# Performance work log

Measured on AMD Instinct MI355X. Metric: run time of the kernel, lower is better.

The kernel has to match this reference:

```python
import jax, jax.numpy as jnp
import numpy as np
from jax import lax

B, T, H, IN = 1024, 100, 512, 4  # batch, seq len (fixed 100 in source), hidden, nucleotide dim


def _lstm_cell(x, h, c, Wih, Whh, b):
    # PyTorch gate order: i, f, g, o ; b = b_ih + b_hh
    gates = x @ Wih.T + h @ Whh.T + b
    i, f, g, o = jnp.split(gates, 4, axis=-1)
    c = jax.nn.sigmoid(f) * c + jax.nn.sigmoid(i) * jnp.tanh(g)
    h = jax.nn.sigmoid(o) * jnp.tanh(c)
    return h, c


def _run_layer(xs, Wih, Whh, b):
    # xs: [T, B, in] -> ys: [T, B, H], final (h, c)
    Bn = xs.shape[1]
    h0 = jnp.zeros((Bn, H), xs.dtype)
    c0 = jnp.zeros((Bn, H), xs.dtype)

    def step(carry, x):
        h, c = carry
        h, c = _lstm_cell(x, h, c, Wih, Whh, b)
        return (h, c), h

    (h, c), ys = lax.scan(step, (h0, c0), xs)
    return ys, h, c


def setup_inputs() -> dict:
    key = jax.random.key(0)
    ks = jax.random.split(key, 16)
    s = lambda fan: 1.0 / np.sqrt(fan)

    def W(k, shape, fan):
        return jax.random.uniform(k, shape, jnp.float32, -s(fan), s(fan))

    inp = {
        "X": jax.random.normal(ks[0], (B, T, IN), jnp.float32),
        "epoch": 10,
        # encoder LSTM (2 layers)
        "enc_Wih0": W(ks[1], (4 * H, IN), H),
        "enc_Whh0": W(ks[2], (4 * H, H), H),
        "enc_b0": jnp.zeros((4 * H,), jnp.float32),
        "enc_Wih1": W(ks[3], (4 * H, H), H),
        "enc_Whh1": W(ks[4], (4 * H, H), H),
        "enc_b1": jnp.zeros((4 * H,), jnp.float32),
        # decoder LSTM (2 layers, input dim = seq_in_dim = 4)
        "dec_Wih0": W(ks[5], (4 * H, IN), H),
        "dec_Whh0": W(ks[6], (4 * H, H), H),
        "dec_b0": jnp.zeros((4 * H,), jnp.float32),
        "dec_Wih1": W(ks[7], (4 * H, H), H),
        "dec_Whh1": W(ks[8], (4 * H, H), H),
        "dec_b1": jnp.zeros((4 * H,), jnp.float32),
        # predict_MLP = Linear(H, 4)
        "Wp": W(ks[9], (IN, H), H),
        "bp": jnp.zeros((IN,), jnp.float32),
    }
    return inp


def reference(X, epoch, enc_Wih0, enc_Whh0, enc_b0, enc_Wih1, enc_Whh1, enc_b1,
              dec_Wih0, dec_Whh0, dec_b0, dec_Wih1, dec_Whh1, dec_b1, Wp, bp):
    # ---- Encoder: 2-layer LSTM over X (batch_first -> scan over time) ----
    xs = jnp.swapaxes(X, 0, 1)  # [T, B, 4]
    ys0, h0e, c0e = _run_layer(xs, enc_Wih0, enc_Whh0, enc_b0)
    _, h1e, c1e = _run_layer(ys0, enc_Wih1, enc_Whh1, enc_b1)

    #      discretize_input=False) ----
    Bn = X.shape[0]
    x_init = jnp.zeros((Bn, IN), X.dtype)

    def dec_step(carry, _):
        x, h0, c0, h1, c1 = carry
        h0, c0 = _lstm_cell(x, h0, c0, dec_Wih0, dec_Whh0, dec_b0)
        h1, c1 = _lstm_cell(h0, h1, c1, dec_Wih1, dec_Whh1, dec_b1)
        pred = h1 @ Wp.T + bp                 # [B, 4] logits
        x_next = jax.nn.softmax(pred, axis=-1)
        return (x_next, h0, c0, h1, c1), pred

    _, preds = lax.scan(dec_step, (x_init, h0e, c0e, h1e, c1e), None, length=T)
    # out_seq list of [B,1,4] in torch -> stacked [B, 100, 4]
    return jnp.swapaxes(preds, 0, 1)
```

## Files before the change

kernel.cpp:

```cpp
#include <hip/hip_runtime.h>
#include <math.h>
#include <stdint.h>

typedef _Float16 f16;
typedef _Float16 f16x8 __attribute__((ext_vector_type(8)));
typedef float f32x4 __attribute__((ext_vector_type(4)));

#define BATCH 1024
#define HD    512
#define TST   100
#define BUFSZ 49152

__device__ __forceinline__ float4 coh_ld_x4(const void* p) {
    float4 v;
    asm volatile("global_load_dwordx4 %0, %1, off sc0 sc1" : "=v"(v) : "v"(p) : "memory");
    return v;
}
__device__ __forceinline__ float4 ld_x4(const void* p) {
    float4 v;
    asm volatile("global_load_dwordx4 %0, %1, off" : "=v"(v) : "v"(p) : "memory");
    return v;
}
__device__ __forceinline__ void coh_store_u32(uint32_t* p, uint32_t v) {
    asm volatile("global_store_dword %0, %1, off sc0 sc1" :: "v"(p), "v"(v) : "memory");
}
__device__ __forceinline__ void coh_store_i32(int* p, int v) {
    asm volatile("global_store_dword %0, %1, off sc0 sc1" :: "v"(p), "v"(v) : "memory");
}
__device__ __forceinline__ int coh_load_i32(const int* p) {
    int v;
    asm volatile("global_load_dword %0, %1, off sc0 sc1\n\ts_waitcnt vmcnt(0)"
                 : "=v"(v) : "v"(p) : "memory");
    return v;
}
__device__ __forceinline__ void drain_vm() {
    asm volatile("s_waitcnt vmcnt(0)" ::: "memory");
    __builtin_amdgcn_sched_barrier(0);
}
__device__ __forceinline__ void wait_vm(int n) {
    switch (n) {
    case 0:  asm volatile("s_waitcnt vmcnt(0)"  ::: "memory"); break;
    case 8:  asm volatile("s_waitcnt vmcnt(8)"  ::: "memory"); break;
    case 12: asm volatile("s_waitcnt vmcnt(12)" ::: "memory"); break;
    case 16: asm volatile("s_waitcnt vmcnt(16)" ::: "memory"); break;
    default: asm volatile("s_waitcnt vmcnt(20)" ::: "memory"); break;
    }
    __builtin_amdgcn_sched_barrier(0);
}

__device__ __forceinline__ float fast_sig(float x) {
    return 1.0f / (1.0f + __expf(-x));
}
__device__ __forceinline__ float fast_tanh(float x) {
    float xc = fminf(fmaxf(x, -15.0f), 15.0f);
    float e = __expf(2.0f * xc);
    return 1.0f - 2.0f / (e + 1.0f);
}

__global__ void split_w(const float* __restrict__ src0, int ksplit,
                        const float* __restrict__ src1, int NKT, f16* __restrict__ out)
{
    int c = blockIdx.x * 256 + threadIdx.x;
    int total = 16 * NKT * 2048;
    if (c >= total) return;
    int u = c & 2047;
    int t2 = c >> 11;
    int kt = t2 % NKT;
    int mt = t2 / NKT;
    int line = u >> 4;
    int s = (u & 15) ^ (line & 15);
    int plane = s >> 3, o = s & 7;
    int m = mt * 128 + line;
    int row = (m & 3) * HD + (m >> 2);
    int kb = kt * 64 + o * 8;
    f16 v[8];
    #pragma unroll
    for (int e = 0; e < 8; ++e) {
        int k = kb + e;
        float w = (k < ksplit) ? src0[(size_t)row * ksplit + k]
                               : src1[(size_t)row * HD + (k - ksplit)];
        float w32 = w * 32.0f;
        f16 hi = (f16)w32;
        v[e] = plane ? (f16)((w32 - (float)hi) * 2048.0f) : hi;
    }
    *(f16x8*)(out + (size_t)c * 8) = *(f16x8*)v;
}

__global__ void prep_b4(const float* __restrict__ b, float* __restrict__ bt) {
    int c = blockIdx.x * 256 + threadIdx.x;
    if (c < 2048) bt[c] = b[(c & 3) * HD + (c >> 2)];
}

__global__ void prep_wih4(const float* __restrict__ W, float* __restrict__ o) {
    int c = blockIdx.x * 256 + threadIdx.x;
    if (c < 8192) {
        int j = c & 3, g = (c >> 2) & 3, hl = c >> 4;
        o[c] = W[(size_t)(g * HD + hl) * 4 + j];
    }
}

__device__ __forceinline__ void publish(int* cell, int epoch) {
    drain_vm();
    __syncthreads();
    if (threadIdx.x == 0)
        coh_store_i32(cell, epoch);
}

__device__ __forceinline__ void wait2(const int* a, int ta, const int* b, int tb) {
    if (threadIdx.x < 64) {
        const int l = threadIdx.x & 15;
        const bool useB = (threadIdx.x & 16) != 0;
        const int* p = (useB ? b : a) + l * 16;
        const int tgt = useB ? tb : ta;
        for (;;) {
            int v = coh_load_i32(p);
            if (__all(v >= tgt)) break;
            __builtin_amdgcn_s_sleep(2);
        }
    }
    __syncthreads();
}

template<int NKT, bool RANK4>
__device__ __forceinline__ void layer_step(
    const f16* __restrict__ Wst, const f16* __restrict__ src1, const f16* __restrict__ src2,
    const float* __restrict__ wih4, const float* __restrict__ xin, int xstride,
    const float* __restrict__ bt4, float* __restrict__ cT, f16* __restrict__ hout,
    char* smem, int mt, int nt)
{
    const int tid = threadIdx.x;
    const int lane = tid & 63;
    const int wv = tid >> 6;
    const int wm = wv & 1, wn = wv >> 1;
    const int l15 = lane & 15, j = lane >> 4;
    const int n0 = nt * 64;

    const int q = (j ^ l15) << 4;
    int ALr[4], BLb[2];
    #pragma unroll
    for (int f = 0; f < 4; ++f) ALr[f] = (wm * 64 + f * 16 + l15) * 256;
    #pragma unroll
    for (int fn = 0; fn < 2; ++fn) BLb[fn] = 32768 + (wn * 32 + fn * 16 + l15) * 256;

    float4 rak[2][8];
    float4 rbk[4][4];
    float4 xv[2];

    auto issueA = [&](int kt, int bank) {
        const f16* ga = Wst + ((size_t)mt * NKT + kt) * 2048 * 8;
        #pragma unroll
        for (int i = 0; i < 8; ++i)
            rak[bank][i] = ld_x4(ga + (size_t)(i * 256 + tid) * 8);
    };
    auto issueB = [&](int kt, int bank) {
        #pragma unroll
        for (int i = 0; i < 4; ++i) {
            int v = i * 256 + tid;
            int line = v >> 4;
            int s = (v & 15) ^ (line & 15);
            int ks = kt * 64 + (s & 7) * 8;
            const f16* sp = src1; int kl = ks;
            if (NKT == 16 && ks >= 512) { sp = src2; kl = ks - 512; }
            rbk[bank][i] = coh_ld_x4(sp + (size_t)(n0 + line) * 1024 + (s >> 3) * 512 + kl);
        }
    };

    f32x4 accA[4][2] = {};
    f32x4 accB[4][2] = {};

    if (RANK4) {
        #pragma unroll
        for (int fn = 0; fn < 2; ++fn) {
            const int n = n0 + wn * 32 + fn * 16 + l15;
            xv[fn] = coh_ld_x4(xin + (size_t)n * xstride);
        }
    }
    issueB(0, 0); issueA(0, 0); issueB(1, 1); issueA(1, 1); issueB(2, 2); issueB(3, 3);

    #pragma unroll
    for (int kt = 0; kt < NKT; ++kt) {
        char* buf = smem + (kt & 1) * BUFSZ;
        const int wcnt = (kt == NKT - 1) ? 0 : (kt == NKT - 2) ? 8 :
                         (kt == NKT - 3) ? 12 : (kt <= 1) ? 20 : 16;
        wait_vm(wcnt);
        #pragma unroll
        for (int i = 0; i < 8; ++i) *(float4*)(buf + (i * 256 + tid) * 16) = rak[kt & 1][i];
        #pragma unroll
        for (int i = 0; i < 4; ++i) *(float4*)(buf + 32768 + (i * 256 + tid) * 16) = rbk[kt & 3][i];
        if (kt + 2 < NKT) issueA(kt + 2, kt & 1);
        if (kt + 4 < NKT) issueB(kt + 4, kt & 3);
        __syncthreads();
        #pragma unroll
        for (int i = 0; i < 2; ++i) {
            const int off = (i << 6) ^ q;
            f16x8 ah[4], al[4], bh[2], bl[2];
            #pragma unroll
            for (int f = 0; f < 4; ++f) {
                ah[f] = *(const f16x8*)(buf + ALr[f] + off);
                al[f] = *(const f16x8*)(buf + ALr[f] + (off ^ 0x80));
            }
            #pragma unroll
            for (int fn = 0; fn < 2; ++fn) {
                bh[fn] = *(const f16x8*)(buf + BLb[fn] + off);
                bl[fn] = *(const f16x8*)(buf + BLb[fn] + (off ^ 0x80));
            }
            #pragma unroll
            for (int f = 0; f < 4; ++f)
                #pragma unroll
                for (int fn = 0; fn < 2; ++fn) {
                    accA[f][fn] = __builtin_amdgcn_mfma_f32_16x16x32_f16(ah[f], bh[fn], accA[f][fn], 0, 0, 0);
                    accB[f][fn] = __builtin_amdgcn_mfma_f32_16x16x32_f16(al[f], bh[fn], accB[f][fn], 0, 0, 0);
                    accB[f][fn] = __builtin_amdgcn_mfma_f32_16x16x32_f16(ah[f], bl[fn], accB[f][fn], 0, 0, 0);
                }
        }
    }

    const float sA = 1.0f / 1024.0f;
    const float sB = 1.0f / (1024.0f * 2048.0f);

    uint32_t* htile = (uint32_t*)smem;
    #pragma unroll
    for (int f = 0; f < 4; ++f) {
        const int hl_loc = wm * 16 + f * 4 + j;
        const int hl = mt * 32 + hl_loc;
        const float4 bv = *(const float4*)(bt4 + hl * 4);
        #pragma unroll
        for (int fn = 0; fn < 2; ++fn) {
            const int n_loc = wn * 32 + fn * 16 + l15;
            const int n = n0 + n_loc;
            float g0 = accA[f][fn][0] * sA + accB[f][fn][0] * sB + bv.x;
            float g1 = accA[f][fn][1] * sA + accB[f][fn][1] * sB + bv.y;
            float g2 = accA[f][fn][2] * sA + accB[f][fn][2] * sB + bv.z;
            float g3 = accA[f][fn][3] * sA + accB[f][fn][3] * sB + bv.w;
            if (RANK4) {
                const float4* wr = (const float4*)(wih4 + hl * 16);
                const float4 x4 = xv[fn];
                g0 += wr[0].x * x4.x + wr[0].y * x4.y + wr[0].z * x4.z + wr[0].w * x4.w;
                g1 += wr[1].x * x4.x + wr[1].y * x4.y + wr[1].z * x4.z + wr[1].w * x4.w;
                g2 += wr[2].x * x4.x + wr[2].y * x4.y + wr[2].z * x4.z + wr[2].w * x4.w;
                g3 += wr[3].x * x4.x + wr[3].y * x4.y + wr[3].z * x4.z + wr[3].w * x4.w;
            }
            const size_t co = (size_t)hl * 1024 + n;
            const float cold = cT[co];
            const float si = fast_sig(g0);
            const float sf = fast_sig(g1);
            const float so = fast_sig(g3);
            const float cn = sf * cold + si * fast_tanh(g2);
            const float hn = so * fast_tanh(cn);
            cT[co] = cn;
            const float h32 = hn * 32.0f;
            const f16 hi = (f16)h32;
            const f16 lo = (f16)((h32 - (float)hi) * 2048.0f);
            uint32_t pk = ((uint32_t)__builtin_bit_cast(uint16_t, lo) << 16)
                        | (uint32_t)__builtin_bit_cast(uint16_t, hi);
            htile[n_loc * 33 + hl_loc] = pk;
        }
    }
    __syncthreads();
    uint32_t* h32out = (uint32_t*)hout;
    #pragma unroll
    for (int i = 0; i < 8; ++i) {
        int u = i * 256 + tid;
        int n_loc = u >> 5;
        int r = u & 31;
        int plane = r >> 4;
        int p = r & 15;
        uint32_t t0 = htile[n_loc * 33 + 2 * p];
        uint32_t t1 = htile[n_loc * 33 + 2 * p + 1];
        uint32_t w = plane ? ((t1 & 0xffff0000u) | (t0 >> 16))
                           : ((t1 << 16) | (t0 & 0xffffu));
        coh_store_u32(h32out + (size_t)(n0 + n_loc) * 512 + plane * 256 + mt * 16 + p, w);
    }
}

__device__ __forceinline__ void pred_step(
    const f16* __restrict__ h1, const float* __restrict__ Wp, const float* __restrict__ bp,
    float* __restrict__ outp, float* __restrict__ xfb, int t, int mt, int nt)
{
    const int lane = threadIdx.x & 63;
    const int wv = threadIdx.x >> 6;
    const int n = nt * 64 + mt * 4 + wv;
    const f16* hr = h1 + (size_t)n * 1024;
    const int k0 = lane * 8;
    float4 hv4 = coh_ld_x4(hr + k0);
    float4 lv4 = coh_ld_x4(hr + 512 + k0);
    drain_vm();
    f16x8 hv = __builtin_bit_cast(f16x8, hv4);
    f16x8 lv = __builtin_bit_cast(f16x8, lv4);
    float h[8];
    #pragma unroll
    for (int e = 0; e < 8; ++e)
        h[e] = (float)hv[e] * 0.03125f + (float)lv[e] * (1.0f / 65536.0f);
    float a[4] = {};
    #pragma unroll
    for (int g = 0; g < 4; ++g) {
        const float4 wa = *(const float4*)(Wp + g * HD + k0);
        const float4 wb = *(const float4*)(Wp + g * HD + k0 + 4);
        a[g] = h[0]*wa.x + h[1]*wa.y + h[2]*wa.z + h[3]*wa.w
             + h[4]*wb.x + h[5]*wb.y + h[6]*wb.z + h[7]*wb.w;
    }
    #pragma unroll
    for (int off = 32; off > 0; off >>= 1) {
        a[0] += __shfl_xor(a[0], off);
        a[1] += __shfl_xor(a[1], off);
        a[2] += __shfl_xor(a[2], off);
        a[3] += __shfl_xor(a[3], off);
    }
    if (lane == 0) {
        const float4 bv = *(const float4*)bp;
        float v0 = a[0] + bv.x, v1 = a[1] + bv.y, v2 = a[2] + bv.z, v3 = a[3] + bv.w;
        float* op = outp + (size_t)n * (TST * 4) + t * 4;
        op[0] = v0; op[1] = v1; op[2] = v2; op[3] = v3;
        float m = fmaxf(fmaxf(v0, v1), fmaxf(v2, v3));
        float e0 = expf(v0 - m), e1 = expf(v1 - m), e2 = expf(v2 - m), e3 = expf(v3 - m);
        float inv = 1.0f / (e0 + e1 + e2 + e3);
        uint32_t* xp = (uint32_t*)(xfb + n * 4);
        float s0 = e0 * inv, s1 = e1 * inv, s2 = e2 * inv, s3 = e3 * inv;
        coh_store_u32(xp + 0, __builtin_bit_cast(uint32_t, s0));
        coh_store_u32(xp + 1, __builtin_bit_cast(uint32_t, s1));
        coh_store_u32(xp + 2, __builtin_bit_cast(uint32_t, s2));
        coh_store_u32(xp + 3, __builtin_bit_cast(uint32_t, s3));
    }
}

struct Params {
    const f16 *WE0, *WE1, *WD0, *WD1;
    const float *wih4E, *wih4D, *btE0, *btE1, *btD0, *btD1;
    const float *X, *Wp, *bp;
    f16 *h0a, *h0b, *h1a, *h1b;
    float *c0, *c1;
    float *xfb0, *xfb1;
    float *out;
    int *f0, *f1, *fp;
};

__launch_bounds__(256, 1) __global__ void lstm_persistent(Params P)
{
    __shared__ __align__(16) char smem[2 * BUFSZ];
    const int bx = blockIdx.x;
    const int mt = ((bx & 7) << 1) | ((bx >> 3) & 1);
    const int nt = bx >> 4;
    int* f0g = P.f0 + nt * 256;
    int* f1g = P.f1 + nt * 256;
    int* fpg = P.fp + nt * 256;
    int* my0 = f0g + mt * 16;
    int* my1 = f1g + mt * 16;
    int* myp = fpg + mt * 16;
    f16* h0b_[2] = { P.h0a, P.h0b };
    f16* h1b_[2] = { P.h1a, P.h1b };
    float* xfb_[2] = { P.xfb0, P.xfb1 };

    for (int u = 0; u < 2 * TST; ++u) {
        const bool enc = (u < TST);
        const int t = enc ? u : u - TST;

        if (enc) wait2(f0g, u, f0g, u);
        else     wait2(f0g, u, fpg, t);
        layer_step<8, true>(enc ? P.WE0 : P.WD0,
                            h0b_[(u + 1) & 1], nullptr,
                            enc ? P.wih4E : P.wih4D,
                            enc ? (P.X + t * 4) : xfb_[(t + 1) & 1],
                            enc ? (TST * 4) : 4,
                            enc ? P.btE0 : P.btD0,
                            P.c0, h0b_[u & 1], smem, mt, nt);
        publish(my0, u + 1);

        wait2(f0g, u + 1, f1g, u);
        layer_step<16, false>(enc ? P.WE1 : P.WD1,
                              h0b_[u & 1], h1b_[(u + 1) & 1],
                              nullptr, nullptr, 0,
                              enc ? P.btE1 : P.btD1,
                              P.c1, h1b_[u & 1], smem, mt, nt);
        publish(my1, u + 1);

        if (!enc) {
            wait2(f1g, u + 1, f1g, u + 1);
            pred_step(h1b_[u & 1], P.Wp, P.bp, P.out, xfb_[t & 1], t, mt, nt);
            publish(myp, t + 1);
        }
    }
}

extern "C" void kernel_launch(void* const* d_in, const int* in_sizes, int n_in,
                              void* d_out, int out_size, void* d_ws, size_t ws_size,
                              hipStream_t stream)
{
    const float* X     = (const float*)d_in[0];
    const float* eWih0 = (const float*)d_in[2];
    const float* eWhh0 = (const float*)d_in[3];
    const float* eb0   = (const float*)d_in[4];
    const float* eWih1 = (const float*)d_in[5];
    const float* eWhh1 = (const float*)d_in[6];
    const float* eb1   = (const float*)d_in[7];
    const float* dWih0 = (const float*)d_in[8];
    const float* dWhh0 = (const float*)d_in[9];
    const float* db0   = (const float*)d_in[10];
    const float* dWih1 = (const float*)d_in[11];
    const float* dWhh1 = (const float*)d_in[12];
    const float* db1   = (const float*)d_in[13];
    const float* Wp    = (const float*)d_in[14];
    const float* bp    = (const float*)d_in[15];

    char* ws = (char*)d_ws;
    size_t off = 0;
    auto alloc = [&](size_t bytes) { char* p = ws + off; off += (bytes + 255) & ~(size_t)255; return p; };
    f16* WE0 = (f16*)alloc((size_t)16 * 8  * 2048 * 16);
    f16* WE1 = (f16*)alloc((size_t)16 * 16 * 2048 * 16);
    f16* WD0 = (f16*)alloc((size_t)16 * 8  * 2048 * 16);
    f16* WD1 = (f16*)alloc((size_t)16 * 16 * 2048 * 16);
    float* wih4E = (float*)alloc(8192 * 4);
    float* wih4D = (float*)alloc(8192 * 4);
    float* btE0 = (float*)alloc(2048 * 4);
    float* btE1 = (float*)alloc(2048 * 4);
    float* btD0 = (float*)alloc(2048 * 4);
    float* btD1 = (float*)alloc(2048 * 4);
    f16* h0a = (f16*)alloc((size_t)BATCH * 1024 * 2);
    f16* h0b = (f16*)alloc((size_t)BATCH * 1024 * 2);
    f16* h1a = (f16*)alloc((size_t)BATCH * 1024 * 2);
    f16* h1b = (f16*)alloc((size_t)BATCH * 1024 * 2);
    float* c0  = (float*)alloc((size_t)HD * BATCH * 4);
    float* c1  = (float*)alloc((size_t)HD * BATCH * 4);
    float* xfb0 = (float*)alloc((size_t)BATCH * 4 * 4);
    float* xfb1 = (float*)alloc((size_t)BATCH * 4 * 4);
    int* f0 = (int*)alloc(16 * 256 * 4);
    int* f1 = (int*)alloc(16 * 256 * 4);
    int* fp = (int*)alloc(16 * 256 * 4);
    if (off > ws_size) return;

    split_w<<<(16 * 8  * 2048) / 256, 256, 0, stream>>>(nullptr, 0,   eWhh0, 8,  WE0);
    split_w<<<(16 * 16 * 2048) / 256, 256, 0, stream>>>(eWih1, 512, eWhh1, 16, WE1);
    split_w<<<(16 * 8  * 2048) / 256, 256, 0, stream>>>(nullptr, 0,   dWhh0, 8,  WD0);
    split_w<<<(16 * 16 * 2048) / 256, 256, 0, stream>>>(dWih1, 512, dWhh1, 16, WD1);
    prep_wih4<<<32, 256, 0, stream>>>(eWih0, wih4E);
    prep_wih4<<<32, 256, 0, stream>>>(dWih0, wih4D);
    prep_b4<<<8, 256, 0, stream>>>(eb0, btE0);
    prep_b4<<<8, 256, 0, stream>>>(eb1, btE1);
    prep_b4<<<8, 256, 0, stream>>>(db0, btD0);
    prep_b4<<<8, 256, 0, stream>>>(db1, btD1);

    hipMemsetAsync(h0b, 0, (size_t)BATCH * 1024 * 2, stream);
    hipMemsetAsync(h1b, 0, (size_t)BATCH * 1024 * 2, stream);
    hipMemsetAsync(c0, 0, (size_t)HD * BATCH * 4, stream);
    hipMemsetAsync(c1, 0, (size_t)HD * BATCH * 4, stream);
    hipMemsetAsync(xfb1, 0, (size_t)BATCH * 4 * 4, stream);
    hipMemsetAsync(f0, 0, 16 * 256 * 4, stream);
    hipMemsetAsync(f1, 0, 16 * 256 * 4, stream);
    hipMemsetAsync(fp, 0, 16 * 256 * 4, stream);

    Params P;
    P.WE0 = WE0; P.WE1 = WE1; P.WD0 = WD0; P.WD1 = WD1;
    P.wih4E = wih4E; P.wih4D = wih4D;
    P.btE0 = btE0; P.btE1 = btE1; P.btD0 = btD0; P.btD1 = btD1;
    P.X = X; P.Wp = Wp; P.bp = bp;
    P.h0a = h0a; P.h0b = h0b; P.h1a = h1a; P.h1b = h1b;
    P.c0 = c0; P.c1 = c1;
    P.xfb0 = xfb0; P.xfb1 = xfb1;
    P.out = (float*)d_out;
    P.f0 = f0; P.f1 = f1; P.fp = fp;

    lstm_persistent<<<256, 256, 0, stream>>>(P);

    (void)in_sizes; (void)n_in; (void)out_size;
}
```

Before: 7.382 ms.

## Retile persistent LSTM to 256x32 tiles with 32x32 MFMA and direct-register weights

Changes the per-block tile from 128 gate rows x 64 batch columns to 256 gate rows x 32 batch columns, using 32x32x16 MFMA instructions. Weight fragments are now loaded from global memory straight into registers in MFMA-ready order, so they no longer pass through shared memory. Only the h operand is staged in a small double-buffered LDS region. Weight pre-layout, flag indexing, the grid mapping and the projection indexing are all rewritten to match. This cuts LDS traffic and LDS footprint per step, but every block now streams twice as many weight rows through registers, and the hand-tuned vmcnt waits must stay exactly right.

```diff
diff --git a/kernel.cpp b/kernel.cpp
--- a/kernel.cpp
+++ b/kernel.cpp
@@ -4,12 +4,11 @@
 
 typedef _Float16 f16;
 typedef _Float16 f16x8 __attribute__((ext_vector_type(8)));
-typedef float f32x4 __attribute__((ext_vector_type(4)));
+typedef float f32x16 __attribute__((ext_vector_type(16)));
 
 #define BATCH 1024
 #define HD    512
 #define TST   100
-#define BUFSZ 49152
 
 __device__ __forceinline__ float4 coh_ld_x4(const void* p) {
     float4 v;
@@ -40,10 +39,12 @@
 __device__ __forceinline__ void wait_vm(int n) {
     switch (n) {
     case 0:  asm volatile("s_waitcnt vmcnt(0)"  ::: "memory"); break;
-    case 8:  asm volatile("s_waitcnt vmcnt(8)"  ::: "memory"); break;
-    case 12: asm volatile("s_waitcnt vmcnt(12)" ::: "memory"); break;
-    case 16: asm volatile("s_waitcnt vmcnt(16)" ::: "memory"); break;
-    default: asm volatile("s_waitcnt vmcnt(20)" ::: "memory"); break;
+    case 4:  asm volatile("s_waitcnt vmcnt(4)"  ::: "memory"); break;
+    case 6:  asm volatile("s_waitcnt vmcnt(6)"  ::: "memory"); break;
+    case 10: asm volatile("s_waitcnt vmcnt(10)" ::: "memory"); break;
+    case 26: asm volatile("s_waitcnt vmcnt(26)" ::: "memory"); break;
+    case 32: asm volatile("s_waitcnt vmcnt(32)" ::: "memory"); break;
+    default: asm volatile("s_waitcnt vmcnt(34)" ::: "memory"); break;
     }
     __builtin_amdgcn_sched_barrier(0);
 }
@@ -61,27 +62,27 @@
                         const float* __restrict__ src1, int NKT, f16* __restrict__ out)
 {
     int c = blockIdx.x * 256 + threadIdx.x;
-    int total = 16 * NKT * 2048;
+    int total = 8 * NKT * 4096;
     if (c >= total) return;
-    int u = c & 2047;
-    int t2 = c >> 11;
+    int q = c & 4095;
+    int t2 = c >> 12;
     int kt = t2 % NKT;
     int mt = t2 / NKT;
-    int line = u >> 4;
-    int s = (u & 15) ^ (line & 15);
-    int plane = s >> 3, o = s & 7;
-    int m = mt * 128 + line;
-    int row = (m & 3) * HD + (m >> 2);
-    int kb = kt * 64 + o * 8;
+    int inner = q >> 8;
+    int row = q & 255;
+    int s = inner >> 2, p = (inner >> 1) & 1, half = inner & 1;
+    int m = mt * 256 + row;
+    int orow = (m & 3) * HD + (m >> 2);
+    int kb = kt * 64 + s * 16 + half * 8;
     f16 v[8];
     #pragma unroll
     for (int e = 0; e < 8; ++e) {
         int k = kb + e;
-        float w = (k < ksplit) ? src0[(size_t)row * ksplit + k]
-                               : src1[(size_t)row * HD + (k - ksplit)];
+        float w = (k < ksplit) ? src0[(size_t)orow * ksplit + k]
+                               : src1[(size_t)orow * HD + (k - ksplit)];
         float w32 = w * 32.0f;
         f16 hi = (f16)w32;
-        v[e] = plane ? (f16)((w32 - (float)hi) * 2048.0f) : hi;
+        v[e] = p ? (f16)((w32 - (float)hi) * 2048.0f) : hi;
     }
     *(f16x8*)(out + (size_t)c * 8) = *(f16x8*)v;
 }
@@ -108,8 +109,8 @@
 
 __device__ __forceinline__ void wait2(const int* a, int ta, const int* b, int tb) {
     if (threadIdx.x < 64) {
-        const int l = threadIdx.x & 15;
-        const bool useB = (threadIdx.x & 16) != 0;
+        const int l = threadIdx.x & 7;
+        const bool useB = (threadIdx.x & 8) != 0;
         const int* p = (useB ? b : a) + l * 16;
         const int tgt = useB ? tb : ta;
         for (;;) {
@@ -128,118 +129,122 @@
     const float* __restrict__ bt4, float* __restrict__ cT, f16* __restrict__ hout,
     char* smem, int mt, int nt)
 {
-    const int tid = threadIdx.x;
+    const int tid  = threadIdx.x;
     const int lane = tid & 63;
-    const int wv = tid >> 6;
-    const int wm = wv & 1, wn = wv >> 1;
-    const int l15 = lane & 15, j = lane >> 4;
-    const int n0 = nt * 64;
-
-    const int q = (j ^ l15) << 4;
-    int ALr[4], BLb[2];
-    #pragma unroll
-    for (int f = 0; f < 4; ++f) ALr[f] = (wm * 64 + f * 16 + l15) * 256;
-    #pragma unroll
-    for (int fn = 0; fn < 2; ++fn) BLb[fn] = 32768 + (wn * 32 + fn * 16 + l15) * 256;
-
-    float4 rak[2][8];
-    float4 rbk[4][4];
-    float4 xv[2];
-
-    auto issueA = [&](int kt, int bank) {
-        const f16* ga = Wst + ((size_t)mt * NKT + kt) * 2048 * 8;
-        #pragma unroll
-        for (int i = 0; i < 8; ++i)
-            rak[bank][i] = ld_x4(ga + (size_t)(i * 256 + tid) * 8);
+    const int wv   = tid >> 6;
+    const int col  = lane & 31;
+    const int half = lane >> 5;
+    const int xk   = lane & 15;
+    const int n0   = nt * 32;
+
+    const size_t tbaseA = (size_t)half * 4096 + (size_t)(wv * 64 + col) * 16;
+    const int colb = col * 256;
+
+    float4 ab0[4], ab1[4], ab2[4], ab3[4];
+    float4 rb0[2], rb1[2];
+    float4 xv = make_float4(0.f, 0.f, 0.f, 0.f);
+
+    auto issueA = [&](int kt, int s, float4 (&bank)[4]) {
+        const char* ga = (const char*)Wst + ((size_t)(mt * NKT + kt) << 16)
+                       + ((size_t)s << 14) + tbaseA;
+        bank[0] = ld_x4(ga);
+        bank[1] = ld_x4(ga + 8192);
+        bank[2] = ld_x4(ga + 512);
+        bank[3] = ld_x4(ga + 8704);
     };
-    auto issueB = [&](int kt, int bank) {
-        #pragma unroll
-        for (int i = 0; i < 4; ++i) {
-            int v = i * 256 + tid;
-            int line = v >> 4;
-            int s = (v & 15) ^ (line & 15);
-            int ks = kt * 64 + (s & 7) * 8;
-            const f16* sp = src1; int kl = ks;
-            if (NKT == 16 && ks >= 512) { sp = src2; kl = ks - 512; }
-            rbk[bank][i] = coh_ld_x4(sp + (size_t)(n0 + line) * 1024 + (s >> 3) * 512 + kl);
-        }
-    };
-
-    f32x4 accA[4][2] = {};
-    f32x4 accB[4][2] = {};
-
-    if (RANK4) {
-        #pragma unroll
-        for (int fn = 0; fn < 2; ++fn) {
-            const int n = n0 + wn * 32 + fn * 16 + l15;
-            xv[fn] = coh_ld_x4(xin + (size_t)n * xstride);
-        }
-    }
-    issueB(0, 0); issueA(0, 0); issueB(1, 1); issueA(1, 1); issueB(2, 2); issueB(3, 3);
-
-    #pragma unroll
-    for (int kt = 0; kt < NKT; ++kt) {
-        char* buf = smem + (kt & 1) * BUFSZ;
-        const int wcnt = (kt == NKT - 1) ? 0 : (kt == NKT - 2) ? 8 :
-                         (kt == NKT - 3) ? 12 : (kt <= 1) ? 20 : 16;
-        wait_vm(wcnt);
-        #pragma unroll
-        for (int i = 0; i < 8; ++i) *(float4*)(buf + (i * 256 + tid) * 16) = rak[kt & 1][i];
-        #pragma unroll
-        for (int i = 0; i < 4; ++i) *(float4*)(buf + 32768 + (i * 256 + tid) * 16) = rbk[kt & 3][i];
-        if (kt + 2 < NKT) issueA(kt + 2, kt & 1);
-        if (kt + 4 < NKT) issueB(kt + 4, kt & 3);
-        __syncthreads();
+    auto issueB = [&](int kt, float4 (&rb)[2]) {
         #pragma unroll
         for (int i = 0; i < 2; ++i) {
-            const int off = (i << 6) ^ q;
-            f16x8 ah[4], al[4], bh[2], bl[2];
-            #pragma unroll
-            for (int f = 0; f < 4; ++f) {
-                ah[f] = *(const f16x8*)(buf + ALr[f] + off);
-                al[f] = *(const f16x8*)(buf + ALr[f] + (off ^ 0x80));
-            }
-            #pragma unroll
-            for (int fn = 0; fn < 2; ++fn) {
-                bh[fn] = *(const f16x8*)(buf + BLb[fn] + off);
-                bl[fn] = *(const f16x8*)(buf + BLb[fn] + (off ^ 0x80));
-            }
-            #pragma unroll
-            for (int f = 0; f < 4; ++f)
-                #pragma unroll
-                for (int fn = 0; fn < 2; ++fn) {
-                    accA[f][fn] = __builtin_amdgcn_mfma_f32_16x16x32_f16(ah[f], bh[fn], accA[f][fn], 0, 0, 0);
-                    accB[f][fn] = __builtin_amdgcn_mfma_f32_16x16x32_f16(al[f], bh[fn], accB[f][fn], 0, 0, 0);
-                    accB[f][fn] = __builtin_amdgcn_mfma_f32_16x16x32_f16(ah[f], bl[fn], accB[f][fn], 0, 0, 0);
-                }
-        }
+            int u = i * 256 + tid;
+            int bc = u >> 4, w16 = u & 15;
+            int si = w16 ^ (bc & 15);
+            int p = si >> 3;
+            int kh = kt * 64 + ((si >> 1) & 3) * 16 + (si & 1) * 8;
+            const f16* sp = src1; int kl = kh;
+            if (NKT == 16 && kh >= 512) { sp = src2; kl = kh - 512; }
+            rb[i] = coh_ld_x4(sp + (size_t)(n0 + bc) * 1024 + p * 512 + kl);
+        }
+    };
+
+    f32x16 accA0 = {}, accA1 = {}, accB0 = {}, accB1 = {};
+
+    if (RANK4) xv = coh_ld_x4(xin + (size_t)(n0 + col) * xstride);
+    issueB(0, rb0);
+    issueB(1, rb1);
+    issueA(0, 0, ab0);
+    issueA(0, 1, ab1);
+
+    #pragma unroll
+    for (int kt = 0; kt < NKT; ++kt) {
+        char* buf = smem + (kt & 1) * 8192;
+        wait_vm(kt == 0 ? 10 : kt == 1 ? 26 : kt == NKT - 1 ? 32 : 34);
+        if ((kt & 1) == 0) {
+            *(float4*)(buf + tid * 16)        = rb0[0];
+            *(float4*)(buf + 4096 + tid * 16) = rb0[1];
+            if (kt + 2 < NKT) issueB(kt + 2, rb0);
+        } else {
+            *(float4*)(buf + tid * 16)        = rb1[0];
+            *(float4*)(buf + 4096 + tid * 16) = rb1[1];
+            if (kt + 2 < NKT) issueB(kt + 2, rb1);
+        }
+        __syncthreads();
+
+        #define KSTEP(S, BK)                                                              \
+        {                                                                                 \
+            f16x8 bh = *(const f16x8*)(buf + colb + ((((S) * 2 + half) ^ xk) << 4));       \
+            f16x8 bl = *(const f16x8*)(buf + colb + (((8 + (S) * 2 + half) ^ xk) << 4));   \
+            f16x8 ah0 = __builtin_bit_cast(f16x8, BK[0]);                                 \
+            f16x8 al0 = __builtin_bit_cast(f16x8, BK[1]);                                 \
+            f16x8 ah1 = __builtin_bit_cast(f16x8, BK[2]);                                 \
+            f16x8 al1 = __builtin_bit_cast(f16x8, BK[3]);                                 \
+            accA0 = __builtin_amdgcn_mfma_f32_32x32x16_f16(ah0, bh, accA0, 0, 0, 0);      \
+            accB0 = __builtin_amdgcn_mfma_f32_32x32x16_f16(al0, bh, accB0, 0, 0, 0);      \
+            accB0 = __builtin_amdgcn_mfma_f32_32x32x16_f16(ah0, bl, accB0, 0, 0, 0);      \
+            accA1 = __builtin_amdgcn_mfma_f32_32x32x16_f16(ah1, bh, accA1, 0, 0, 0);      \
+            accB1 = __builtin_amdgcn_mfma_f32_32x32x16_f16(al1, bh, accB1, 0, 0, 0);      \
+            accB1 = __builtin_amdgcn_mfma_f32_32x32x16_f16(ah1, bl, accB1, 0, 0, 0);      \
+        }
+
+        wait_vm(kt >= NKT - 2 ? 4 : 6);
+        KSTEP(0, ab0)
+        issueA(kt, 2, ab2);
+        wait_vm(kt >= NKT - 2 ? 4 : 6);
+        KSTEP(1, ab1)
+        issueA(kt, 3, ab3);
+        wait_vm(4);
+        KSTEP(2, ab2)
+        if (kt + 1 < NKT) issueA(kt + 1, 0, ab0);
+        wait_vm(kt == NKT - 1 ? 0 : 4);
+        KSTEP(3, ab3)
+        if (kt + 1 < NKT) issueA(kt + 1, 1, ab1);
+        #undef KSTEP
     }
 
     const float sA = 1.0f / 1024.0f;
     const float sB = 1.0f / (1024.0f * 2048.0f);
-
-    uint32_t* htile = (uint32_t*)smem;
-    #pragma unroll
-    for (int f = 0; f < 4; ++f) {
-        const int hl_loc = wm * 16 + f * 4 + j;
-        const int hl = mt * 32 + hl_loc;
-        const float4 bv = *(const float4*)(bt4 + hl * 4);
+    uint32_t* htile = (uint32_t*)(smem + 16384);
+
+    #pragma unroll
+    for (int f = 0; f < 2; ++f) {
+        const f32x16 aA = f ? accA1 : accA0;
+        const f32x16 aB = f ? accB1 : accB0;
         #pragma unroll
-        for (int fn = 0; fn < 2; ++fn) {
-            const int n_loc = wn * 32 + fn * 16 + l15;
-            const int n = n0 + n_loc;
-            float g0 = accA[f][fn][0] * sA + accB[f][fn][0] * sB + bv.x;
-            float g1 = accA[f][fn][1] * sA + accB[f][fn][1] * sB + bv.y;
-            float g2 = accA[f][fn][2] * sA + accB[f][fn][2] * sB + bv.z;
-            float g3 = accA[f][fn][3] * sA + accB[f][fn][3] * sB + bv.w;
+        for (int qq = 0; qq < 4; ++qq) {
+            const int hl_loc = wv * 16 + f * 8 + 2 * qq + half;
+            const int hl = mt * 64 + hl_loc;
+            const float4 bv = *(const float4*)(bt4 + hl * 4);
+            float g0 = aA[4 * qq + 0] * sA + aB[4 * qq + 0] * sB + bv.x;
+            float g1 = aA[4 * qq + 1] * sA + aB[4 * qq + 1] * sB + bv.y;
+            float g2 = aA[4 * qq + 2] * sA + aB[4 * qq + 2] * sB + bv.z;
+            float g3 = aA[4 * qq + 3] * sA + aB[4 * qq + 3] * sB + bv.w;
             if (RANK4) {
                 const float4* wr = (const float4*)(wih4 + hl * 16);
-                const float4 x4 = xv[fn];
-                g0 += wr[0].x * x4.x + wr[0].y * x4.y + wr[0].z * x4.z + wr[0].w * x4.w;
-                g1 += wr[1].x * x4.x + wr[1].y * x4.y + wr[1].z * x4.z + wr[1].w * x4.w;
-                g2 += wr[2].x * x4.x + wr[2].y * x4.y + wr[2].z * x4.z + wr[2].w * x4.w;
-                g3 += wr[3].x * x4.x + wr[3].y * x4.y + wr[3].z * x4.z + wr[3].w * x4.w;
+                g0 += wr[0].x * xv.x + wr[0].y * xv.y + wr[0].z * xv.z + wr[0].w * xv.w;
+                g1 += wr[1].x * xv.x + wr[1].y * xv.y + wr[1].z * xv.z + wr[1].w * xv.w;
+                g2 += wr[2].x * xv.x + wr[2].y * xv.y + wr[2].z * xv.z + wr[2].w * xv.w;
+                g3 += wr[3].x * xv.x + wr[3].y * xv.y + wr[3].z * xv.z + wr[3].w * xv.w;
             }
+            const int n = n0 + col;
             const size_t co = (size_t)hl * 1024 + n;
             const float cold = cT[co];
             const float si = fast_sig(g0);
@@ -248,28 +253,28 @@
             const float cn = sf * cold + si * fast_tanh(g2);
             const float hn = so * fast_tanh(cn);
             cT[co] = cn;
-            const float h32 = hn * 32.0f;
-            const f16 hi = (f16)h32;
-            const f16 lo = (f16)((h32 - (float)hi) * 2048.0f);
+            const float h32v = hn * 32.0f;
+            const f16 hi = (f16)h32v;
+            const f16 lo = (f16)((h32v - (float)hi) * 2048.0f);
             uint32_t pk = ((uint32_t)__builtin_bit_cast(uint16_t, lo) << 16)
                         | (uint32_t)__builtin_bit_cast(uint16_t, hi);
-            htile[n_loc * 33 + hl_loc] = pk;
+            htile[col * 65 + hl_loc] = pk;
         }
     }
     __syncthreads();
     uint32_t* h32out = (uint32_t*)hout;
     #pragma unroll
-    for (int i = 0; i < 8; ++i) {
-        int u = i * 256 + tid;
-        int n_loc = u >> 5;
-        int r = u & 31;
-        int plane = r >> 4;
-        int p = r & 15;
-        uint32_t t0 = htile[n_loc * 33 + 2 * p];
-        uint32_t t1 = htile[n_loc * 33 + 2 * p + 1];
-        uint32_t w = plane ? ((t1 & 0xffff0000u) | (t0 >> 16))
+    for (int e = 0; e < 8; ++e) {
+        int u = e * 256 + tid;
+        int cc = u >> 6;
+        int rem = u & 63;
+        int pl = rem >> 5;
+        int w = rem & 31;
+        uint32_t t0 = htile[cc * 65 + 2 * w];
+        uint32_t t1 = htile[cc * 65 + 2 * w + 1];
+        uint32_t word = pl ? ((t1 & 0xffff0000u) | (t0 >> 16))
                            : ((t1 << 16) | (t0 & 0xffffu));
-        coh_store_u32(h32out + (size_t)(n0 + n_loc) * 512 + plane * 256 + mt * 16 + p, w);
+        coh_store_u32(h32out + (size_t)(n0 + cc) * 512 + pl * 256 + mt * 32 + w, word);
     }
 }
 
@@ -279,7 +284,7 @@
 {
     const int lane = threadIdx.x & 63;
     const int wv = threadIdx.x >> 6;
-    const int n = nt * 64 + mt * 4 + wv;
+    const int n = nt * 32 + mt * 4 + wv;
     const f16* hr = h1 + (size_t)n * 1024;
     const int k0 = lane * 8;
     float4 hv4 = coh_ld_x4(hr + k0);
@@ -336,13 +341,13 @@
 
 __launch_bounds__(256, 1) __global__ void lstm_persistent(Params P)
 {
-    __shared__ __align__(16) char smem[2 * BUFSZ];
+    __shared__ __align__(16) char smem[16384 + 8448];
     const int bx = blockIdx.x;
-    const int mt = ((bx & 7) << 1) | ((bx >> 3) & 1);
-    const int nt = bx >> 4;
-    int* f0g = P.f0 + nt * 256;
-    int* f1g = P.f1 + nt * 256;
-    int* fpg = P.fp + nt * 256;
+    const int mt = bx & 7;
+    const int nt = bx >> 3;
+    int* f0g = P.f0 + nt * 128;
+    int* f1g = P.f1 + nt * 128;
+    int* fpg = P.fp + nt * 128;
     int* my0 = f0g + mt * 16;
     int* my1 = f1g + mt * 16;
     int* myp = fpg + mt * 16;
@@ -404,10 +409,10 @@
     char* ws = (char*)d_ws;
     size_t off = 0;
     auto alloc = [&](size_t bytes) { char* p = ws + off; off += (bytes + 255) & ~(size_t)255; return p; };
-    f16* WE0 = (f16*)alloc((size_t)16 * 8  * 2048 * 16);
-    f16* WE1 = (f16*)alloc((size_t)16 * 16 * 2048 * 16);
-    f16* WD0 = (f16*)alloc((size_t)16 * 8  * 2048 * 16);
-    f16* WD1 = (f16*)alloc((size_t)16 * 16 * 2048 * 16);
+    f16* WE0 = (f16*)alloc((size_t)8 * 8  * 65536);
+    f16* WE1 = (f16*)alloc((size_t)8 * 16 * 65536);
+    f16* WD0 = (f16*)alloc((size_t)8 * 8  * 65536);
+    f16* WD1 = (f16*)alloc((size_t)8 * 16 * 65536);
     float* wih4E = (float*)alloc(8192 * 4);
     float* wih4D = (float*)alloc(8192 * 4);
     float* btE0 = (float*)alloc(2048 * 4);
@@ -422,15 +427,15 @@
     float* c1  = (float*)alloc((size_t)HD * BATCH * 4);
     float* xfb0 = (float*)alloc((size_t)BATCH * 4 * 4);
     float* xfb1 = (float*)alloc((size_t)BATCH * 4 * 4);
-    int* f0 = (int*)alloc(16 * 256 * 4);
-    int* f1 = (int*)alloc(16 * 256 * 4);
-    int* fp = (int*)alloc(16 * 256 * 4);
+    int* f0 = (int*)alloc(32 * 128 * 4);
+    int* f1 = (int*)alloc(32 * 128 * 4);
+    int* fp = (int*)alloc(32 * 128 * 4);
     if (off > ws_size) return;
 
-    split_w<<<(16 * 8  * 2048) / 256, 256, 0, stream>>>(nullptr, 0,   eWhh0, 8,  WE0);
-    split_w<<<(16 * 16 * 2048) / 256, 256, 0, stream>>>(eWih1, 512, eWhh1, 16, WE1);
-    split_w<<<(16 * 8  * 2048) / 256, 256, 0, stream>>>(nullptr, 0,   dWhh0, 8,  WD0);
-    split_w<<<(16 * 16 * 2048) / 256, 256, 0, stream>>>(dWih1, 512, dWhh1, 16, WD1);
+    split_w<<<(8 * 8  * 4096) / 256, 256, 0, stream>>>(nullptr, 0,   eWhh0, 8,  WE0);
+    split_w<<<(8 * 16 * 4096) / 256, 256, 0, stream>>>(eWih1, 512, eWhh1, 16, WE1);
+    split_w<<<(8 * 8  * 4096) / 256, 256, 0, stream>>>(nullptr, 0,   dWhh0, 8,  WD0);
+    split_w<<<(8 * 16 * 4096) / 256, 256, 0, stream>>>(dWih1, 512, dWhh1, 16, WD1);
     prep_wih4<<<32, 256, 0, stream>>>(eWih0, wih4E);
     prep_wih4<<<32, 256, 0, stream>>>(dWih0, wih4D);
     prep_b4<<<8, 256, 0, stream>>>(eb0, btE0);
@@ -443,9 +448,9 @@
     hipMemsetAsync(c0, 0, (size_t)HD * BATCH * 4, stream);
     hipMemsetAsync(c1, 0, (size_t)HD * BATCH * 4, stream);
     hipMemsetAsync(xfb1, 0, (size_t)BATCH * 4 * 4, stream);
-    hipMemsetAsync(f0, 0, 16 * 256 * 4, stream);
-    hipMemsetAsync(f1, 0, 16 * 256 * 4, stream);
-    hipMemsetAsync(fp, 0, 16 * 256 * 4, stream);
+    hipMemsetAsync(f0, 0, 32 * 128 * 4, stream);
+    hipMemsetAsync(f1, 0, 32 * 128 * 4, stream);
+    hipMemsetAsync(fp, 0, 32 * 128 * 4, stream);
 
     Params P;
     P.WE0 = WE0; P.WE1 = WE1; P.WD0 = WD0; P.WD1 = WD1;
```

Measured after the change: 7.458 ms. No clear change (+1.0%).

## Halve batch tile and K-chunk to run 512 persistent blocks at two per CU

Applied to the files above, without the earlier changes.

Each persistent block now covers 32 batch columns instead of 64 and walks K in 32-wide chunks instead of 64. The weight staging layout, shared buffers and prefetch depth shrink to match, and the grid doubles to 512 blocks with two resident per CU. The goal is more parallelism and latency hiding across CUs for the serial recurrent steps. In exchange each weight tile is streamed twice as often, the flag arrays grow, and more blocks take part in every grid-wide synchronisation.

```diff
diff --git a/kernel.cpp b/kernel.cpp
--- a/kernel.cpp
+++ b/kernel.cpp
@@ -9,7 +9,7 @@
 #define BATCH 1024
 #define HD    512
 #define TST   100
-#define BUFSZ 49152
+#define BUFSZ 20480
 
 __device__ __forceinline__ float4 coh_ld_x4(const void* p) {
     float4 v;
@@ -38,13 +38,8 @@
     __builtin_amdgcn_sched_barrier(0);
 }
 __device__ __forceinline__ void wait_vm(int n) {
-    switch (n) {
-    case 0:  asm volatile("s_waitcnt vmcnt(0)"  ::: "memory"); break;
-    case 8:  asm volatile("s_waitcnt vmcnt(8)"  ::: "memory"); break;
-    case 12: asm volatile("s_waitcnt vmcnt(12)" ::: "memory"); break;
-    case 16: asm volatile("s_waitcnt vmcnt(16)" ::: "memory"); break;
-    default: asm volatile("s_waitcnt vmcnt(20)" ::: "memory"); break;
-    }
+    if (n == 0) asm volatile("s_waitcnt vmcnt(0)" ::: "memory");
+    else        asm volatile("s_waitcnt vmcnt(5)" ::: "memory");
     __builtin_amdgcn_sched_barrier(0);
 }
 
@@ -61,24 +56,24 @@
                         const float* __restrict__ src1, int NKT, f16* __restrict__ out)
 {
     int c = blockIdx.x * 256 + threadIdx.x;
-    int total = 16 * NKT * 2048;
+    int total = 16 * NKT * 1024;
     if (c >= total) return;
-    int u = c & 2047;
-    int t2 = c >> 11;
+    int u = c & 1023;
+    int t2 = c >> 10;
     int kt = t2 % NKT;
     int mt = t2 / NKT;
-    int line = u >> 4;
-    int s = (u & 15) ^ (line & 15);
-    int plane = s >> 3, o = s & 7;
+    int line = u >> 3, pos = u & 7;
+    int s = pos ^ (line & 7);
+    int plane = s >> 2, o = s & 3;
     int m = mt * 128 + line;
-    int row = (m & 3) * HD + (m >> 2);
-    int kb = kt * 64 + o * 8;
+    int orow = (m & 3) * HD + (m >> 2);
+    int kb = kt * 32 + o * 8;
     f16 v[8];
     #pragma unroll
     for (int e = 0; e < 8; ++e) {
         int k = kb + e;
-        float w = (k < ksplit) ? src0[(size_t)row * ksplit + k]
-                               : src1[(size_t)row * HD + (k - ksplit)];
+        float w = (k < ksplit) ? src0[(size_t)orow * ksplit + k]
+                               : src1[(size_t)orow * HD + (k - ksplit)];
         float w32 = w * 32.0f;
         f16 hi = (f16)w32;
         v[e] = plane ? (f16)((w32 - (float)hi) * 2048.0f) : hi;
@@ -105,7 +100,6 @@
     if (threadIdx.x == 0)
         coh_store_i32(cell, epoch);
 }
-
 __device__ __forceinline__ void wait2(const int* a, int ta, const int* b, int tb) {
     if (threadIdx.x < 64) {
         const int l = threadIdx.x & 15;
@@ -128,148 +122,121 @@
     const float* __restrict__ bt4, float* __restrict__ cT, f16* __restrict__ hout,
     char* smem, int mt, int nt)
 {
-    const int tid = threadIdx.x;
+    const int tid  = threadIdx.x;
     const int lane = tid & 63;
-    const int wv = tid >> 6;
-    const int wm = wv & 1, wn = wv >> 1;
-    const int l15 = lane & 15, j = lane >> 4;
-    const int n0 = nt * 64;
-
-    const int q = (j ^ l15) << 4;
-    int ALr[4], BLb[2];
-    #pragma unroll
-    for (int f = 0; f < 4; ++f) ALr[f] = (wm * 64 + f * 16 + l15) * 256;
-    #pragma unroll
-    for (int fn = 0; fn < 2; ++fn) BLb[fn] = 32768 + (wn * 32 + fn * 16 + l15) * 256;
-
-    float4 rak[2][8];
-    float4 rbk[4][4];
-    float4 xv[2];
-
-    auto issueA = [&](int kt, int bank) {
-        const f16* ga = Wst + ((size_t)mt * NKT + kt) * 2048 * 8;
+    const int wv   = tid >> 6;
+    const int wm   = wv & 1, wn = wv >> 1;
+    const int l15  = lane & 15, j = lane >> 4;
+    const int n0   = nt * 32;
+    const int key  = (j ^ (l15 & 7)) << 4;
+
+    int ALr[4];
+    #pragma unroll
+    for (int f = 0; f < 4; ++f) ALr[f] = (wm * 64 + f * 16 + l15) * 128;
+    const int BLb = 16384 + (wn * 16 + l15) * 128;
+
+    float4 ra0[4], ra1[4];
+    float4 rb0, rb1;
+    float4 xv = make_float4(0.f, 0.f, 0.f, 0.f);
+
+    auto issueA = [&](int kt, float4 (&ra)[4]) {
+        const f16* ga = Wst + ((size_t)(mt * NKT + kt)) * 8192;
         #pragma unroll
-        for (int i = 0; i < 8; ++i)
-            rak[bank][i] = ld_x4(ga + (size_t)(i * 256 + tid) * 8);
+        for (int i = 0; i < 4; ++i)
+            ra[i] = ld_x4(ga + (size_t)(i * 256 + tid) * 8);
     };
-    auto issueB = [&](int kt, int bank) {
-        #pragma unroll
-        for (int i = 0; i < 4; ++i) {
-            int v = i * 256 + tid;
-            int line = v >> 4;
-            int s = (v & 15) ^ (line & 15);
-            int ks = kt * 64 + (s & 7) * 8;
-            const f16* sp = src1; int kl = ks;
-            if (NKT == 16 && ks >= 512) { sp = src2; kl = ks - 512; }
-            rbk[bank][i] = coh_ld_x4(sp + (size_t)(n0 + line) * 1024 + (s >> 3) * 512 + kl);
-        }
+    auto issueB = [&](int kt, float4& rb) {
+        int bc = tid >> 3, pos = tid & 7;
+        int si = pos ^ (bc & 7);
+        int plane = si >> 2;
+        int kh = kt * 32 + (si & 3) * 8;
+        const f16* sp = src1; int kl = kh;
+        if (NKT == 32 && kh >= 512) { sp = src2; kl = kh - 512; }
+        rb = coh_ld_x4(sp + (size_t)(n0 + bc) * 1024 + plane * 512 + kl);
     };
 
-    f32x4 accA[4][2] = {};
-    f32x4 accB[4][2] = {};
-
-    if (RANK4) {
-        #pragma unroll
-        for (int fn = 0; fn < 2; ++fn) {
-            const int n = n0 + wn * 32 + fn * 16 + l15;
-            xv[fn] = coh_ld_x4(xin + (size_t)n * xstride);
-        }
-    }
-    issueB(0, 0); issueA(0, 0); issueB(1, 1); issueA(1, 1); issueB(2, 2); issueB(3, 3);
+    f32x4 accA[4] = {};
+    f32x4 accB[4] = {};
+
+    if (RANK4) xv = coh_ld_x4(xin + (size_t)(n0 + wn * 16 + l15) * xstride);
+    issueB(0, rb0); issueA(0, ra0); issueB(1, rb1); issueA(1, ra1);
 
     #pragma unroll
     for (int kt = 0; kt < NKT; ++kt) {
         char* buf = smem + (kt & 1) * BUFSZ;
-        const int wcnt = (kt == NKT - 1) ? 0 : (kt == NKT - 2) ? 8 :
-                         (kt == NKT - 3) ? 12 : (kt <= 1) ? 20 : 16;
-        wait_vm(wcnt);
+        wait_vm(kt == NKT - 1 ? 0 : 5);
+        const float4* rap = (kt & 1) ? ra1 : ra0;
         #pragma unroll
-        for (int i = 0; i < 8; ++i) *(float4*)(buf + (i * 256 + tid) * 16) = rak[kt & 1][i];
+        for (int i = 0; i < 4; ++i)
+            *(float4*)(buf + (i * 256 + tid) * 16) = rap[i];
+        *(float4*)(buf + 16384 + tid * 16) = (kt & 1) ? rb1 : rb0;
+        if (kt + 2 < NKT) {
+            if ((kt & 1) == 0) { issueB(kt + 2, rb0); issueA(kt + 2, ra0); }
+            else               { issueB(kt + 2, rb1); issueA(kt + 2, ra1); }
+        }
+        __syncthreads();
+        f16x8 bh = *(const f16x8*)(buf + BLb + key);
+        f16x8 bl = *(const f16x8*)(buf + BLb + (key ^ 0x40));
         #pragma unroll
-        for (int i = 0; i < 4; ++i) *(float4*)(buf + 32768 + (i * 256 + tid) * 16) = rbk[kt & 3][i];
-        if (kt + 2 < NKT) issueA(kt + 2, kt & 1);
-        if (kt + 4 < NKT) issueB(kt + 4, kt & 3);
-        __syncthreads();
-        #pragma unroll
-        for (int i = 0; i < 2; ++i) {
-            const int off = (i << 6) ^ q;
-            f16x8 ah[4], al[4], bh[2], bl[2];
-            #pragma unroll
-            for (int f = 0; f < 4; ++f) {
-                ah[f] = *(const f16x8*)(buf + ALr[f] + off);
-                al[f] = *(const f16x8*)(buf + ALr[f] + (off ^ 0x80));
-            }
-            #pragma unroll
-            for (int fn = 0; fn < 2; ++fn) {
-                bh[fn] = *(const f16x8*)(buf + BLb[fn] + off);
-                bl[fn] = *(const f16x8*)(buf + BLb[fn] + (off ^ 0x80));
-            }
-            #pragma unroll
-            for (int f = 0; f < 4; ++f)
-                #pragma unroll
-                for (int fn = 0; fn < 2; ++fn) {
-                    accA[f][fn] = __builtin_amdgcn_mfma_f32_16x16x32_f16(ah[f], bh[fn], accA[f][fn], 0, 0, 0);
-                    accB[f][fn] = __builtin_amdgcn_mfma_f32_16x16x32_f16(al[f], bh[fn], accB[f][fn], 0, 0, 0);
-                    accB[f][fn] = __builtin_amdgcn_mfma_f32_16x16x32_f16(ah[f], bl[fn], accB[f][fn], 0, 0, 0);
-                }
+        for (int f = 0; f < 4; ++f) {
+            f16x8 ah = *(const f16x8*)(buf + ALr[f] + key);
+            f16x8 al = *(const f16x8*)(buf + ALr[f] + (key ^ 0x40));
+            accA[f] = __builtin_amdgcn_mfma_f32_16x16x32_f16(ah, bh, accA[f], 0, 0, 0);
+            accB[f] = __builtin_amdgcn_mfma_f32_16x16x32_f16(al, bh, accB[f], 0, 0, 0);
+            accB[f] = __builtin_amdgcn_mfma_f32_16x16x32_f16(ah, bl, accB[f], 0, 0, 0);
         }
     }
 
     const float sA = 1.0f / 1024.0f;
     const float sB = 1.0f / (1024.0f * 2048.0f);
-
-    uint32_t* htile = (uint32_t*)smem;
+    uint32_t* htile = (uint32_t*)(smem + 2 * BUFSZ);
     #pragma unroll
     for (int f = 0; f < 4; ++f) {
         const int hl_loc = wm * 16 + f * 4 + j;
         const int hl = mt * 32 + hl_loc;
         const float4 bv = *(const float4*)(bt4 + hl * 4);
-        #pragma unroll
-        for (int fn = 0; fn < 2; ++fn) {
-            const int n_loc = wn * 32 + fn * 16 + l15;
-            const int n = n0 + n_loc;
-            float g0 = accA[f][fn][0] * sA + accB[f][fn][0] * sB + bv.x;
-            float g1 = accA[f][fn][1] * sA + accB[f][fn][1] * sB + bv.y;
-            float g2 = accA[f][fn][2] * sA + accB[f][fn][2] * sB + bv.z;
-            float g3 = accA[f][fn][3] * sA + accB[f][fn][3] * sB + bv.w;
-            if (RANK4) {
-                const float4* wr = (const float4*)(wih4 + hl * 16);
-                const float4 x4 = xv[fn];
-                g0 += wr[0].x * x4.x + wr[0].y * x4.y + wr[0].z * x4.z + wr[0].w * x4.w;
-                g1 += wr[1].x * x4.x + wr[1].y * x4.y + wr[1].z * x4.z + wr[1].w * x4.w;
-                g2 += wr[2].x * x4.x + wr[2].y * x4.y + wr[2].z * x4.z + wr[2].w * x4.w;
-                g3 += wr[3].x * x4.x + wr[3].y * x4.y + wr[3].z * x4.z + wr[3].w * x4.w;
-            }
-            const size_t co = (size_t)hl * 1024 + n;
-            const float cold = cT[co];
-            const float si = fast_sig(g0);
-            const float sf = fast_sig(g1);
-            const float so = fast_sig(g3);
-            const float cn = sf * cold + si * fast_tanh(g2);
-            const float hn = so * fast_tanh(cn);
-            cT[co] = cn;
-            const float h32 = hn * 32.0f;
-            const f16 hi = (f16)h32;
-            const f16 lo = (f16)((h32 - (float)hi) * 2048.0f);
-            uint32_t pk = ((uint32_t)__builtin_bit_cast(uint16_t, lo) << 16)
-                        | (uint32_t)__builtin_bit_cast(uint16_t, hi);
-            htile[n_loc * 33 + hl_loc] = pk;
+        const int n_loc = wn * 16 + l15;
+        const int n = n0 + n_loc;
+        float g0 = accA[f][0] * sA + accB[f][0] * sB + bv.x;
+        float g1 = accA[f][1] * sA + accB[f][1] * sB + bv.y;
+        float g2 = accA[f][2] * sA + accB[f][2] * sB + bv.z;
+        float g3 = accA[f][3] * sA + accB[f][3] * sB + bv.w;
+        if (RANK4) {
+            const float4* wr = (const float4*)(wih4 + hl * 16);
+            g0 += wr[0].x * xv.x + wr[0].y * xv.y + wr[0].z * xv.z + wr[0].w * xv.w;
+            g1 += wr[1].x * xv.x + wr[1].y * xv.y + wr[1].z * xv.z + wr[1].w * xv.w;
+            g2 += wr[2].x * xv.x + wr[2].y * xv.y + wr[2].z * xv.z + wr[2].w * xv.w;
+            g3 += wr[3].x * xv.x + wr[3].y * xv.y + wr[3].z * xv.z + wr[3].w * xv.w;
         }
+        const size_t co = (size_t)hl * 1024 + n;
+        const float cold = cT[co];
+        const float si = fast_sig(g0);
+        const float sf = fast_sig(g1);
+        const float so = fast_sig(g3);
+        const float cn = sf * cold + si * fast_tanh(g2);
+        const float hn = so * fast_tanh(cn);
+        cT[co] = cn;
+        const float h32v = hn * 32.0f;
+        const f16 hi = (f16)h32v;
+        const f16 lo = (f16)((h32v - (float)hi) * 2048.0f);
+        uint32_t pk = ((uint32_t)__builtin_bit_cast(uint16_t, lo) << 16)
+                    | (uint32_t)__builtin_bit_cast(uint16_t, hi);
+        htile[n_loc * 33 + hl_loc] = pk;
     }
     __syncthreads();
     uint32_t* h32out = (uint32_t*)hout;
     #pragma unroll
-    for (int i = 0; i < 8; ++i) {
+    for (int i = 0; i < 4; ++i) {
         int u = i * 256 + tid;
-        int n_loc = u >> 5;
-        int r = u & 31;
-        int plane = r >> 4;
-        int p = r & 15;
-        uint32_t t0 = htile[n_loc * 33 + 2 * p];
-        uint32_t t1 = htile[n_loc * 33 + 2 * p + 1];
-        uint32_t w = plane ? ((t1 & 0xffff0000u) | (t0 >> 16))
+        int cc = u >> 5;
+        int rem = u & 31;
+        int pl = rem >> 4;
+        int w = rem & 15;
+        uint32_t t0 = htile[cc * 33 + 2 * w];
+        uint32_t t1 = htile[cc * 33 + 2 * w + 1];
+        uint32_t word = pl ? ((t1 & 0xffff0000u) | (t0 >> 16))
                            : ((t1 << 16) | (t0 & 0xffffu));
-        coh_store_u32(h32out + (size_t)(n0 + n_loc) * 512 + plane * 256 + mt * 16 + p, w);
+        coh_store_u32(h32out + (size_t)(n0 + cc) * 512 + pl * 256 + mt * 16 + w, word);
     }
 }
 
@@ -279,7 +246,8 @@
 {
     const int lane = threadIdx.x & 63;
     const int wv = threadIdx.x >> 6;
-    const int n = nt * 64 + mt * 4 + wv;
+    if (wv >= 2) return;
+    const int n = nt * 32 + mt * 2 + wv;
     const f16* hr = h1 + (size_t)n * 1024;
     const int k0 = lane * 8;
     float4 hv4 = coh_ld_x4(hr + k0);
@@ -334,9 +302,9 @@
     int *f0, *f1, *fp;
 };
 
-__launch_bounds__(256, 1) __global__ void lstm_persistent(Params P)
+__launch_bounds__(256, 2) __global__ void lstm_persistent(Params P)
 {
-    __shared__ __align__(16) char smem[2 * BUFSZ];
+    __shared__ __align__(16) char smem[2 * BUFSZ + 4224];
     const int bx = blockIdx.x;
     const int mt = ((bx & 7) << 1) | ((bx >> 3) & 1);
     const int nt = bx >> 4;
@@ -356,17 +324,17 @@
 
         if (enc) wait2(f0g, u, f0g, u);
         else     wait2(f0g, u, fpg, t);
-        layer_step<8, true>(enc ? P.WE0 : P.WD0,
-                            h0b_[(u + 1) & 1], nullptr,
-                            enc ? P.wih4E : P.wih4D,
-                            enc ? (P.X + t * 4) : xfb_[(t + 1) & 1],
-                            enc ? (TST * 4) : 4,
-                            enc ? P.btE0 : P.btD0,
-                            P.c0, h0b_[u & 1], smem, mt, nt);
+        layer_step<16, true>(enc ? P.WE0 : P.WD0,
+                             h0b_[(u + 1) & 1], nullptr,
+                             enc ? P.wih4E : P.wih4D,
+                             enc ? (P.X + t * 4) : xfb_[(t + 1) & 1],
+                             enc ? (TST * 4) : 4,
+                             enc ? P.btE0 : P.btD0,
+                             P.c0, h0b_[u & 1], smem, mt, nt);
         publish(my0, u + 1);
 
         wait2(f0g, u + 1, f1g, u);
-        layer_step<16, false>(enc ? P.WE1 : P.WD1,
+        layer_step<32, false>(enc ? P.WE1 : P.WD1,
                               h0b_[u & 1], h1b_[(u + 1) & 1],
                               nullptr, nullptr, 0,
                               enc ? P.btE1 : P.btD1,
@@ -404,10 +372,10 @@
     char* ws = (char*)d_ws;
     size_t off = 0;
     auto alloc = [&](size_t bytes) { char* p = ws + off; off += (bytes + 255) & ~(size_t)255; return p; };
-    f16* WE0 = (f16*)alloc((size_t)16 * 8  * 2048 * 16);
-    f16* WE1 = (f16*)alloc((size_t)16 * 16 * 2048 * 16);
-    f16* WD0 = (f16*)alloc((size_t)16 * 8  * 2048 * 16);
-    f16* WD1 = (f16*)alloc((size_t)16 * 16 * 2048 * 16);
+    f16* WE0 = (f16*)alloc((size_t)16 * 16 * 16384);
+    f16* WE1 = (f16*)alloc((size_t)16 * 32 * 16384);
+    f16* WD0 = (f16*)alloc((size_t)16 * 16 * 16384);
+    f16* WD1 = (f16*)alloc((size_t)16 * 32 * 16384);
     float* wih4E = (float*)alloc(8192 * 4);
     float* wih4D = (float*)alloc(8192 * 4);
     float* btE0 = (float*)alloc(2048 * 4);
@@ -422,15 +390,15 @@
     float* c1  = (float*)alloc((size_t)HD * BATCH * 4);
     float* xfb0 = (float*)alloc((size_t)BATCH * 4 * 4);
     float* xfb1 = (float*)alloc((size_t)BATCH * 4 * 4);
-    int* f0 = (int*)alloc(16 * 256 * 4);
-    int* f1 = (int*)alloc(16 * 256 * 4);
-    int* fp = (int*)alloc(16 * 256 * 4);
+    int* f0 = (int*)alloc(32 * 256 * 4);
+    int* f1 = (int*)alloc(32 * 256 * 4);
+    int* fp = (int*)alloc(32 * 256 * 4);
     if (off > ws_size) return;
 
-    split_w<<<(16 * 8  * 2048) / 256, 256, 0, stream>>>(nullptr, 0,   eWhh0, 8,  WE0);
-    split_w<<<(16 * 16 * 2048) / 256, 256, 0, stream>>>(eWih1, 512, eWhh1, 16, WE1);
-    split_w<<<(16 * 8  * 2048) / 256, 256, 0, stream>>>(nullptr, 0,   dWhh0, 8,  WD0);
-    split_w<<<(16 * 16 * 2048) / 256, 256, 0, stream>>>(dWih1, 512, dWhh1, 16, WD1);
+    split_w<<<(16 * 16 * 1024) / 256, 256, 0, stream>>>(nullptr, 0,   eWhh0, 16, WE0);
+    split_w<<<(16 * 32 * 1024) / 256, 256, 0, stream>>>(eWih1, 512, eWhh1, 32, WE1);
+    split_w<<<(16 * 16 * 1024) / 256, 256, 0, stream>>>(nullptr, 0,   dWhh0, 16, WD0);
+    split_w<<<(16 * 32 * 1024) / 256, 256, 0, stream>>>(dWih1, 512, dWhh1, 32, WD1);
     prep_wih4<<<32, 256, 0, stream>>>(eWih0, wih4E);
     prep_wih4<<<32, 256, 0, stream>>>(dWih0, wih4D);
     prep_b4<<<8, 256, 0, stream>>>(eb0, btE0);
@@ -443,9 +411,9 @@
     hipMemsetAsync(c0, 0, (size_t)HD * BATCH * 4, stream);
     hipMemsetAsync(c1, 0, (size_t)HD * BATCH * 4, stream);
     hipMemsetAsync(xfb1, 0, (size_t)BATCH * 4 * 4, stream);
-    hipMemsetAsync(f0, 0, 16 * 256 * 4, stream);
-    hipMemsetAsync(f1, 0, 16 * 256 * 4, stream);
-    hipMemsetAsync(fp, 0, 16 * 256 * 4, stream);
+    hipMemsetAsync(f0, 0, 32 * 256 * 4, stream);
+    hipMemsetAsync(f1, 0, 32 * 256 * 4, stream);
+    hipMemsetAsync(fp, 0, 32 * 256 * 4, stream);
 
     Params P;
     P.WE0 = WE0; P.WE1 = WE1; P.WD0 = WD0; P.WD1 = WD1;
@@ -458,7 +426,7 @@
     P.out = (float*)d_out;
     P.f0 = f0; P.f1 = f1; P.fp = fp;
 
-    lstm_persistent<<<256, 256, 0, stream>>>(P);
+    lstm_persistent<<<512, 256, 0, stream>>>(P);
 
     (void)in_sizes; (void)n_in; (void)out_size;
 }
```

Result: slower. 7.765 ms (+5.2%).
